# Kernel optimization log

Measured on AMD Instinct MI355X. Metric: run time of the kernel, lower is better.

Reference implementation:

```python
import jax, jax.numpy as jnp
import numpy as np
from jax import lax

CONF_THRESH = 0.01
IOU_THRESH = 0.45
TOP_K = 200
NMS_MAX = 400        # nms_max_output_size
NMS_CAND = 512       # candidates kept per class before greedy NMS (fixed-shape cap)
IMG_H = 512.0
IMG_W = 512.0
BATCH, N_BOXES, N_CLASSES = 32, 8732, 81  # last dim = N_CLASSES + 12


def setup_inputs() -> dict:
    key = jax.random.key(0)
    y_pred = jax.random.uniform(key, (BATCH, N_BOXES, N_CLASSES + 12), dtype=jnp.float32)
    return {"y_pred": y_pred}


def _decode_boxes(y):
    # centroids decode: offsets * variances * anchors + anchor centers
    anchor_w = y[..., -6]
    anchor_h = y[..., -5]
    cx = y[..., -12] * y[..., -4] * anchor_w + y[..., -8]
    cy = y[..., -11] * y[..., -3] * anchor_h + y[..., -7]
    w = jnp.exp(y[..., -10] * y[..., -2]) * anchor_w
    h = jnp.exp(y[..., -9] * y[..., -1]) * anchor_h
    xmin = (cx - 0.5 * w) * IMG_W  # normalize_coords=True -> scale to absolute
    ymin = (cy - 0.5 * h) * IMG_H
    xmax = (cx + 0.5 * w) * IMG_W
    ymax = (cy + 0.5 * h) * IMG_H
    return jnp.stack([xmin, ymin, xmax, ymax], axis=-1)  # (B,N,4)


def _iou(box, boxes):
    # box: (...,1,4) vs boxes: (...,K,4), coords [xmin,ymin,xmax,ymax]
    ix1 = jnp.maximum(box[..., 0], boxes[..., 0])
    iy1 = jnp.maximum(box[..., 1], boxes[..., 1])
    ix2 = jnp.minimum(box[..., 2], boxes[..., 2])
    iy2 = jnp.minimum(box[..., 3], boxes[..., 3])
    inter = jnp.maximum(ix2 - ix1, 0.0) * jnp.maximum(iy2 - iy1, 0.0)
    area_a = (box[..., 2] - box[..., 0]) * (box[..., 3] - box[..., 1])
    area_b = (boxes[..., 2] - boxes[..., 0]) * (boxes[..., 3] - boxes[..., 1])
    union = area_a + area_b - inter
    return jnp.where(union > 0, inter / union, 0.0)


def _forward(y_pred):
    B, N, D = y_pred.shape
    C = D - 12 - 1  # foreground classes (class 0 = background is skipped)
    K = NMS_CAND
    boxes = _decode_boxes(y_pred)                        # (B,N,4)
    scores = jnp.swapaxes(y_pred[..., 1:D - 12], 1, 2)   # (B,C,N)
    valid = scores > CONF_THRESH

    # sort candidates per (batch, class) by score desc; invalid go last
    order = jnp.argsort(jnp.where(valid, -scores, jnp.inf), axis=-1)[..., :K]
    s_s = jnp.take_along_axis(scores, order, axis=-1)            # (B,C,K)
    v_s = jnp.take_along_axis(valid, order, axis=-1)             # (B,C,K)
    boxes_bc = jnp.broadcast_to(boxes[:, None], (B, C, N, 4))
    b_s = jnp.take_along_axis(boxes_bc, order[..., None], axis=2)  # (B,C,K,4)

    # greedy NMS over sorted candidates, batched over (B,C)
    def step(carry, x):
        suppressed, count = carry  # (B,C,K) bool, (B,C) int32
        v_i, box_i, i = x
        sup_i = lax.dynamic_index_in_dim(suppressed, i, axis=2, keepdims=False)
        keep = v_i & ~sup_i & (count < NMS_MAX)
        iou = _iou(box_i[:, :, None, :], b_s)            # (B,C,K)
        later = jnp.arange(K) > i
        suppressed = suppressed | (keep[..., None] & (iou > IOU_THRESH) & later)
        return (suppressed, count + keep.astype(jnp.int32)), keep

    init = (jnp.zeros((B, C, K), bool), jnp.zeros((B, C), jnp.int32))
    xs = (jnp.moveaxis(v_s, 2, 0), jnp.moveaxis(b_s, 2, 0), jnp.arange(K))
    _, keeps = lax.scan(step, init, xs)
    keep = jnp.moveaxis(keeps, 0, 2)  # (B,C,K)

    # rows: [class_id, confidence, xmin, ymin, xmax, ymax]
    cls_ids = jnp.broadcast_to((jnp.arange(C, dtype=jnp.float32) + 1.0)[None, :, None], (B, C, K))
    entries = jnp.concatenate([cls_ids[..., None], s_s[..., None], b_s], axis=-1)  # (B,C,K,6)

    # compact kept rows to the front of each class block, zero-pad to NMS_MAX
    pos = jnp.where(keep, jnp.cumsum(keep, axis=-1) - 1, NMS_MAX)  # OOB -> dropped
    bb = jnp.arange(B)[:, None, None]
    cc = jnp.arange(C)[None, :, None]
    padded = jnp.zeros((B, C, NMS_MAX, 6), jnp.float32).at[bb, cc, pos].set(entries, mode='drop')

    flat = padded.reshape(B, C * NMS_MAX, 6)
    _, idx = lax.top_k(flat[:, :, 1], TOP_K)
    return jnp.take_along_axis(flat, idx[:, :, None], axis=1)  # (B, TOP_K, 6)


def reference(y_pred):
    return _forward(y_pred)
```

## Files before the change

kernel.cpp:

```cpp
#include <hip/hip_runtime.h>
#include <stdint.h>


#define BATCH   32
#define NBOX    8732
#define NCH     93
#define NCLS    80
#define KSEL    512
#define NMSMAX  400
#define RPC     200
#define TOPK    200
#define CONF    0.01f
#define IOU_T   0.45f
#define NPT     35

#define M_IOU   0.45000000298023223876953125

typedef unsigned long long u64;
typedef unsigned int       u32;

__device__ __forceinline__ u32 forder(float f) {
  u32 u = __float_as_uint(f);
  return u ^ ((u >> 31) ? 0xFFFFFFFFu : 0x80000000u);
}

template<int NN, int T>
__device__ void bsort(u64* s, int tid, bool asc) {
  for (int k = 2; k <= NN; k <<= 1) {
    for (int j = k >> 1; j > 0; j >>= 1) {
      __syncthreads();
      for (int i = tid; i < NN; i += T) {
        int p = i ^ j;
        if (p > i) {
          u64 a = s[i], b = s[p];
          bool up = (((i & k) == 0) == asc);
          if (up ? (a > b) : (a < b)) { s[i] = b; s[p] = a; }
        }
      }
    }
  }
  __syncthreads();
}

template<int NN, int T>
__device__ void bmerge_asc(u64* s, int tid) {
  for (int j = NN >> 1; j > 0; j >>= 1) {
    __syncthreads();
    for (int i = tid; i < NN; i += T) {
      int p = i ^ j;
      if (p > i) {
        u64 a = s[i], b = s[p];
        if (a > b) { s[i] = b; s[p] = a; }
      }
    }
  }
  __syncthreads();
}

__global__ __launch_bounds__(256) void decode_transpose(
    const float* __restrict__ y, float4* __restrict__ boxes, float* __restrict__ scoresT) {
  __shared__ float tile[64 * NCH];
  int b  = blockIdx.x;
  int t0 = blockIdx.y * 64;
  int nn = NBOX - t0; if (nn > 64) nn = 64;
  const float* src = y + ((size_t)b * NBOX + t0) * NCH;
  int tid = threadIdx.x;
  for (int i = tid; i < nn * NCH; i += 256) tile[i] = src[i];
  __syncthreads();
  if (tid < nn) {
    const float* yy = &tile[tid * NCH];
    float aw = yy[87], ah = yy[88];
    float cx = __fadd_rn(__fmul_rn(__fmul_rn(yy[81], yy[89]), aw), yy[85]);
    float cy = __fadd_rn(__fmul_rn(__fmul_rn(yy[82], yy[90]), ah), yy[86]);
    float w  = __fmul_rn(expf(__fmul_rn(yy[83], yy[91])), aw);
    float h  = __fmul_rn(expf(__fmul_rn(yy[84], yy[92])), ah);
    float4 bx;
    bx.x = __fmul_rn(__fsub_rn(cx, __fmul_rn(0.5f, w)), 512.0f);
    bx.y = __fmul_rn(__fsub_rn(cy, __fmul_rn(0.5f, h)), 512.0f);
    bx.z = __fmul_rn(__fadd_rn(cx, __fmul_rn(0.5f, w)), 512.0f);
    bx.w = __fmul_rn(__fadd_rn(cy, __fmul_rn(0.5f, h)), 512.0f);
    boxes[(size_t)b * NBOX + t0 + tid] = bx;
  }
  for (int e = tid; e < NCLS * 64; e += 256) {
    int c = e >> 6, ln = e & 63;
    if (ln < nn)
      scoresT[((size_t)b * NCLS + c) * NBOX + t0 + ln] = tile[ln * NCH + 1 + c];
  }
}

__global__ __launch_bounds__(256) void select_top512(
    const float* __restrict__ scoresT, u64* __restrict__ selkeys) {
  __shared__ u32 hist[256];
  __shared__ u64 cand[1024];
  __shared__ u32 bcast[4];
  int bc  = blockIdx.x;
  int t   = threadIdx.x;
  const float* sc = scoresT + (size_t)bc * NBOX;
  int base = t * NPT;
  int cnt  = NBOX - base; cnt = cnt < 0 ? 0 : (cnt > NPT ? NPT : cnt);

  u32 khi[NPT];
  #pragma unroll
  for (int k = 0; k < NPT; ++k) {
    float s = (k < cnt) ? sc[base + k] : 0.0f;
    u32 f = forder(s);
    khi[k] = ((k < cnt) && (s > CONF)) ? ~f : 0xFFFFFFFFu;
  }

  u32 prefix = 0, cntLess = 0, cntTie = 0;
  int shift = 24, p;
  for (p = 0; p < 4; ++p) {
    shift = 24 - 8 * p;
    __syncthreads();
    hist[t] = 0;
    __syncthreads();
    #pragma unroll
    for (int k = 0; k < NPT; ++k) {
      u32 x = khi[k];
      bool match = (p == 0) || ((x >> (shift + 8)) == prefix);
      if (match) atomicAdd(&hist[(x >> shift) & 0xFFu], 1u);
    }
    __syncthreads();
    if (t < 64) {
      u32 h0 = hist[4*t], h1 = hist[4*t+1], h2 = hist[4*t+2], h3 = hist[4*t+3];
      u32 lsum = h0 + h1 + h2 + h3;
      u32 scn = lsum;
      #pragma unroll
      for (int d = 1; d < 64; d <<= 1) {
        u32 v = __shfl_up(scn, d, 64);
        if (t >= d) scn += v;
      }
      u32 before = scn - lsum;
      u32 need = 512u - cntLess;
      u32 c0 = before + h0, c1 = c0 + h1, c2 = c1 + h2, c3 = c2 + h3;
      int bin = -1; u32 cb = 0;
      if (before < need) {
        if      (c0 >= need) { bin = 4*t;     cb = before; }
        else if (c1 >= need) { bin = 4*t + 1; cb = c0; }
        else if (c2 >= need) { bin = 4*t + 2; cb = c1; }
        else if (c3 >= need) { bin = 4*t + 3; cb = c2; }
      }
      if (bin >= 0) { bcast[0] = (u32)bin; bcast[1] = cb; }
    }
    __syncthreads();
    u32 bin = bcast[0];
    prefix  = (prefix << 8) | bin;
    cntLess += bcast[1];
    cntTie  = hist[bin];
    if (cntLess + cntTie <= 1024u) break;
  }

  if (p < 4) {
    __syncthreads();
    if (t == 0) bcast[2] = 0;
    __syncthreads();
    #pragma unroll
    for (int k = 0; k < NPT; ++k) {
      u32 x = khi[k];
      if ((x >> shift) <= prefix) {
        u32 pos = atomicAdd(&bcast[2], 1u);
        cand[pos] = ((u64)x << 32) | (u32)(base + k);
      }
    }
    __syncthreads();
    u32 m = bcast[2];
    for (int i = t; i < 1024; i += 256) if (i >= (int)m) cand[i] = ~0ULL;
    bsort<1024, 256>(cand, t, true);
    for (int i = t; i < KSEL; i += 256) selkeys[(size_t)bc * KSEL + i] = cand[i];
  } else {
    u32 V = prefix;
    __syncthreads();
    if (t == 0) bcast[2] = 0;
    __syncthreads();
    #pragma unroll
    for (int k = 0; k < NPT; ++k) {
      u32 x = khi[k];
      if (x < V) {
        u32 pos = atomicAdd(&bcast[2], 1u);
        cand[pos] = ((u64)x << 32) | (u32)(base + k);
      }
    }
    __syncthreads();
    u32 m = bcast[2];
    for (int i = t; i < 512; i += 256) if (i >= (int)m) cand[i] = ~0ULL;
    bsort<512, 256>(cand, t, true);
    for (int i = t; i < (int)m; i += 256) selkeys[(size_t)bc * KSEL + i] = cand[i];
    u32 myeq = 0;
    #pragma unroll
    for (int k = 0; k < NPT; ++k) if (khi[k] == V) myeq++;
    __syncthreads();
    hist[t] = myeq;
    __syncthreads();
    for (int d = 1; d < 256; d <<= 1) {
      u32 v = hist[t];
      u32 w = (t >= d) ? hist[t - d] : 0u;
      __syncthreads();
      hist[t] = v + w;
      __syncthreads();
    }
    u32 r = hist[t] - myeq;
    u32 needEq = 512u - m;
    #pragma unroll
    for (int k = 0; k < NPT; ++k) {
      if (khi[k] == V) {
        if (r < needEq)
          selkeys[(size_t)bc * KSEL + m + r] = ((u64)V << 32) | (u32)(base + k);
        r++;
      }
    }
  }
}

__global__ __launch_bounds__(256) void nms(
    const u64* __restrict__ selkeys, const float4* __restrict__ boxes,
    float* __restrict__ rows, u64* __restrict__ keys) {
  __shared__ float4 sbox[KSEL];
  __shared__ float  sarea[KSEL];
  __shared__ float  sscore[KSEL];
  __shared__ unsigned char svalid[KSEL];
  __shared__ u64   cmat[64][8];
  __shared__ short skidx[RPC];
  __shared__ int   s_gcount;
  int bc = blockIdx.x;
  int b = bc / NCLS, c = bc % NCLS;
  int tid = threadIdx.x;

  for (int i = tid; i < KSEL; i += 256) {
    u64 k  = selkeys[(size_t)bc * KSEL + i];
    u32 khi = (u32)(k >> 32);
    u32 idx = (u32)k;
    bool val = (khi != 0xFFFFFFFFu);
    u32 x = ~khi;
    u32 bits = (x & 0x80000000u) ? (x ^ 0x80000000u) : ~x;
    sscore[i] = __uint_as_float(bits);
    svalid[i] = val ? 1 : 0;
    float4 bx = make_float4(0.f, 0.f, 0.f, 0.f);
    if (val && idx < NBOX) bx = boxes[(size_t)b * NBOX + idx];
    sbox[i] = bx;
    sarea[i] = __fmul_rn(__fsub_rn(bx.z, bx.x), __fsub_rn(bx.w, bx.y));
  }
  if (tid == 0) s_gcount = 0;
  __syncthreads();

  u64 keptm[8] = {0,0,0,0,0,0,0,0};

  #pragma unroll
  for (int T = 0; T < 8; ++T) {
    bool active = (s_gcount < RPC);
    if (active) {
      for (int task = tid; task < 64 * (T + 1); task += 256) {
        int jl = task & 63, wi = task >> 6;
        int j = T * 64 + jl;
        float4 bj = sbox[j];
        float ab = sarea[j];
        u64 m = 0;
        for (int ii = 0; ii < 64; ++ii) {
          int i = wi * 64 + ii;
          float4 bi = sbox[i];
          float aa = sarea[i];
          float ix1 = fmaxf(bi.x, bj.x);
          float iy1 = fmaxf(bi.y, bj.y);
          float ix2 = fminf(bi.z, bj.z);
          float iy2 = fminf(bi.w, bj.w);
          float iw = fmaxf(__fsub_rn(ix2, ix1), 0.f);
          float ih = fmaxf(__fsub_rn(iy2, iy1), 0.f);
          float inter = __fmul_rn(iw, ih);
          float un = __fsub_rn(__fadd_rn(aa, ab), inter);
          bool s = (un > 0.f) && ((double)inter > M_IOU * (double)un);
          m |= ((u64)(s ? 1u : 0u)) << ii;
        }
        cmat[jl][wi] = m;
      }
    }
    __syncthreads();
    if (active && tid < 64) {
      int lane = tid;
      u64 cm[8];
      #pragma unroll
      for (int w = 0; w < 8; ++w) cm[w] = (w <= T) ? cmat[lane][w] : 0ull;
      int count = s_gcount;
      u64 hit = 0;
      #pragma unroll
      for (int w = 0; w < 8; ++w) hit |= cm[w] & keptm[w];
      bool valb = (svalid[T * 64 + lane] != 0);
      u64 alive = __ballot(valb && (hit == 0ull));
      while (alive != 0ull && count < RPC) {
        int i = __ffsll(alive) - 1;
        if (lane == i) skidx[count] = (short)(T * 64 + i);
        keptm[T] |= (1ull << i);
        alive &= ~(1ull << i);
        count++;
        if (count >= RPC) break;
        bool ks = ((cm[T] >> i) & 1ull) != 0ull;
        alive &= ~__ballot(ks);
      }
      if (lane == 0) s_gcount = count;
    }
    __syncthreads();
  }

  int count = s_gcount;
  for (int r = tid; r < RPC; r += 256) {
    float* row = rows + ((size_t)bc * RPC + r) * 6;
    u64 k;
    if (r < count) {
      int i = skidx[r];
      float s = sscore[i];
      float4 bx = sbox[i];
      row[0] = (float)(c + 1); row[1] = s;
      row[2] = bx.x; row[3] = bx.y; row[4] = bx.z; row[5] = bx.w;
      k = ((u64)(~forder(s)) << 32) | (u32)(c * NMSMAX + r);
    } else {
      row[0] = 0.f; row[1] = 0.f; row[2] = 0.f; row[3] = 0.f; row[4] = 0.f; row[5] = 0.f;
      k = ((u64)0x7FFFFFFFu << 32) | (u32)(c * NMSMAX + r);
    }
    keys[(size_t)bc * RPC + r] = k;
  }
}

__global__ __launch_bounds__(256) void topk_l1(
    const u64* __restrict__ keys, u64* __restrict__ out1) {
  __shared__ u64 buf[256], chk[256];
  int b = blockIdx.x, g = blockIdx.y;
  const u64* kb = keys + (size_t)b * (NCLS * RPC) + (size_t)g * (8 * RPC);
  int tid = threadIdx.x;
  buf[tid] = kb[tid];
  bsort<256, 256>(buf, tid, true);
  for (int c0 = 256; c0 < 1792; c0 += 256) {
    int n = c0 + tid;
    chk[tid] = (n < 8 * RPC) ? kb[n] : ~0ULL;
    bsort<256, 256>(chk, tid, false);
    u64 a = buf[tid], bb = chk[tid];
    buf[tid] = (a < bb) ? a : bb;
    bmerge_asc<256, 256>(buf, tid);
  }
  out1[((size_t)b * 10 + g) * 256 + tid] = buf[tid];
}

__global__ __launch_bounds__(256) void topk_l2(
    const u64* __restrict__ out1, const float* __restrict__ rows, float* __restrict__ out) {
  __shared__ u64 buf[256], chk[256];
  int b = blockIdx.x;
  const u64* kb = out1 + (size_t)b * 2560;
  int tid = threadIdx.x;
  buf[tid] = kb[tid];
  bsort<256, 256>(buf, tid, true);
  for (int c0 = 256; c0 < 2560; c0 += 256) {
    chk[tid] = kb[c0 + tid];
    bsort<256, 256>(chk, tid, false);
    u64 a = buf[tid], bb = chk[tid];
    buf[tid] = (a < bb) ? a : bb;
    bmerge_asc<256, 256>(buf, tid);
  }
  if (tid < TOPK) {
    u64 k = buf[tid];
    u32 f = (u32)k;
    float* o = out + ((size_t)b * TOPK + tid) * 6;
    if (f == 0xFFFFFFFFu) {
      o[0]=0.f; o[1]=0.f; o[2]=0.f; o[3]=0.f; o[4]=0.f; o[5]=0.f;
    } else {
      u32 c = f / NMSMAX;
      u32 r = f % NMSMAX;
      const float* row = rows + (((size_t)b * NCLS + c) * RPC + r) * 6;
      o[0]=row[0]; o[1]=row[1]; o[2]=row[2]; o[3]=row[3]; o[4]=row[4]; o[5]=row[5];
    }
  }
}

extern "C" void kernel_launch(void* const* d_in, const int* in_sizes, int n_in,
                              void* d_out, int out_size, void* d_ws, size_t ws_size,
                              hipStream_t stream) {
  (void)in_sizes; (void)n_in; (void)out_size; (void)ws_size;
  const float* y = (const float*)d_in[0];
  float* out = (float*)d_out;
  char* ws = (char*)d_ws;

  constexpr size_t OFF_BOXES   = 0;
  constexpr size_t SZ_BOXES    = (size_t)BATCH * NBOX * 4 * 4;
  constexpr size_t OFF_SCORES  = OFF_BOXES + SZ_BOXES;
  constexpr size_t SZ_SCORES   = (size_t)BATCH * NCLS * NBOX * 4;
  constexpr size_t OFF_SELKEYS = OFF_SCORES + SZ_SCORES;
  constexpr size_t SZ_SELKEYS  = (size_t)BATCH * NCLS * KSEL * 8;
  constexpr size_t OFF_ROWS    = OFF_SELKEYS + SZ_SELKEYS;
  constexpr size_t SZ_ROWS     = (size_t)BATCH * NCLS * RPC * 6 * 4;
  constexpr size_t OFF_KEYS    = OFF_ROWS + SZ_ROWS;
  constexpr size_t SZ_KEYS     = (size_t)BATCH * NCLS * RPC * 8;
  constexpr size_t OFF_OUT1    = OFF_KEYS + SZ_KEYS;

  float4* boxes  = (float4*)(ws + OFF_BOXES);
  float* scoresT = (float*)(ws + OFF_SCORES);
  u64* selkeys   = (u64*)(ws + OFF_SELKEYS);
  float* rows    = (float*)(ws + OFF_ROWS);
  u64* keys      = (u64*)(ws + OFF_KEYS);
  u64* out1      = (u64*)(ws + OFF_OUT1);

  dim3 gA(BATCH, (NBOX + 63) / 64);
  decode_transpose<<<gA, 256, 0, stream>>>(y, boxes, scoresT);
  select_top512<<<BATCH * NCLS, 256, 0, stream>>>(scoresT, selkeys);
  nms<<<BATCH * NCLS, 256, 0, stream>>>(selkeys, boxes, rows, keys);
  dim3 gD1(BATCH, 10);
  topk_l1<<<gD1, 256, 0, stream>>>(keys, out1);
  topk_l2<<<BATCH, 256, 0, stream>>>(out1, rows, out);
}
```

Measured before the change: 691.9 us.

## Check NMS candidates only against kept boxes instead of full IoU matrix

Reworks the per-class NMS block. Each 64-candidate tile is now tested only against the already-kept boxes, split across four waves and combined by ballot, plus a 64x64 intra-tile IoU mask built in 16-bit chunks. Previously each tile computed IoU against every earlier candidate. Box data moves from float4 to structure-of-arrays in shared memory, and the loop exits early once 200 boxes are kept. This cuts IoU work from quadratic in candidates to roughly candidates times kept boxes, but the loop over kept boxes is serial and uneven across waves.

```diff
diff --git a/kernel.cpp b/kernel.cpp
--- a/kernel.cpp
+++ b/kernel.cpp
@@ -22,6 +22,20 @@
 __device__ __forceinline__ u32 forder(float f) {
   u32 u = __float_as_uint(f);
   return u ^ ((u >> 31) ? 0xFFFFFFFFu : 0x80000000u);
+}
+
+__device__ __forceinline__ bool iou_gt(
+    float kx, float ky, float kz, float kw, float aa,
+    float bx, float by, float bz, float bw, float ab) {
+  float ix1 = fmaxf(kx, bx);
+  float iy1 = fmaxf(ky, by);
+  float ix2 = fminf(kz, bz);
+  float iy2 = fminf(kw, bw);
+  float iw = fmaxf(__fsub_rn(ix2, ix1), 0.f);
+  float ih = fmaxf(__fsub_rn(iy2, iy1), 0.f);
+  float inter = __fmul_rn(iw, ih);
+  float un = __fsub_rn(__fadd_rn(aa, ab), inter);
+  return (un > 0.f) && ((double)inter > M_IOU * (double)un);
 }
 
 template<int NN, int T>
@@ -214,13 +228,12 @@
 __global__ __launch_bounds__(256) void nms(
     const u64* __restrict__ selkeys, const float4* __restrict__ boxes,
     float* __restrict__ rows, u64* __restrict__ keys) {
-  __shared__ float4 sbox[KSEL];
-  __shared__ float  sarea[KSEL];
-  __shared__ float  sscore[KSEL];
+  __shared__ float sx[KSEL], sy[KSEL], sz[KSEL], sw_[KSEL], sa[KSEL], ss[KSEL];
   __shared__ unsigned char svalid[KSEL];
-  __shared__ u64   cmat[64][8];
   __shared__ short skidx[RPC];
   __shared__ int   s_gcount;
+  __shared__ u64   ssup[4];
+  __shared__ u32   scmat[64][5];
   int bc = blockIdx.x;
   int b = bc / NCLS, c = bc % NCLS;
   int tid = threadIdx.x;
@@ -232,69 +245,60 @@
     bool val = (khi != 0xFFFFFFFFu);
     u32 x = ~khi;
     u32 bits = (x & 0x80000000u) ? (x ^ 0x80000000u) : ~x;
-    sscore[i] = __uint_as_float(bits);
+    ss[i] = __uint_as_float(bits);
     svalid[i] = val ? 1 : 0;
     float4 bx = make_float4(0.f, 0.f, 0.f, 0.f);
     if (val && idx < NBOX) bx = boxes[(size_t)b * NBOX + idx];
-    sbox[i] = bx;
-    sarea[i] = __fmul_rn(__fsub_rn(bx.z, bx.x), __fsub_rn(bx.w, bx.y));
+    sx[i] = bx.x; sy[i] = bx.y; sz[i] = bx.z; sw_[i] = bx.w;
+    sa[i] = __fmul_rn(__fsub_rn(bx.z, bx.x), __fsub_rn(bx.w, bx.y));
   }
   if (tid == 0) s_gcount = 0;
   __syncthreads();
 
-  u64 keptm[8] = {0,0,0,0,0,0,0,0};
-
-  #pragma unroll
+  int jl = tid & 63, wv = tid >> 6;
   for (int T = 0; T < 8; ++T) {
-    bool active = (s_gcount < RPC);
-    if (active) {
-      for (int task = tid; task < 64 * (T + 1); task += 256) {
-        int jl = task & 63, wi = task >> 6;
-        int j = T * 64 + jl;
-        float4 bj = sbox[j];
-        float ab = sarea[j];
-        u64 m = 0;
-        for (int ii = 0; ii < 64; ++ii) {
-          int i = wi * 64 + ii;
-          float4 bi = sbox[i];
-          float aa = sarea[i];
-          float ix1 = fmaxf(bi.x, bj.x);
-          float iy1 = fmaxf(bi.y, bj.y);
-          float ix2 = fminf(bi.z, bj.z);
-          float iy2 = fminf(bi.w, bj.w);
-          float iw = fmaxf(__fsub_rn(ix2, ix1), 0.f);
-          float ih = fmaxf(__fsub_rn(iy2, iy1), 0.f);
-          float inter = __fmul_rn(iw, ih);
-          float un = __fsub_rn(__fadd_rn(aa, ab), inter);
-          bool s = (un > 0.f) && ((double)inter > M_IOU * (double)un);
-          m |= ((u64)(s ? 1u : 0u)) << ii;
-        }
-        cmat[jl][wi] = m;
-      }
-    }
-    __syncthreads();
-    if (active && tid < 64) {
+    int count = s_gcount;
+    if (count >= RPC) break;
+    int j = T * 64 + jl;
+    float bjx = sx[j], bjy = sy[j], bjz = sz[j], bjw = sw_[j], ab = sa[j];
+
+    bool supA = false;
+    for (int r = wv; r < count; r += 4) {
+      int ki = skidx[r];
+      if (iou_gt(sx[ki], sy[ki], sz[ki], sw_[ki], sa[ki], bjx, bjy, bjz, bjw, ab))
+        supA = true;
+    }
+    u64 bwm = __ballot(supA);
+    if (jl == 0) ssup[wv] = bwm;
+
+    u32 mchunk = 0;
+    #pragma unroll
+    for (int k = 0; k < 16; ++k) {
+      int i = T * 64 + wv * 16 + k;
+      bool s = iou_gt(sx[i], sy[i], sz[i], sw_[i], sa[i], bjx, bjy, bjz, bjw, ab);
+      mchunk |= (s ? 1u : 0u) << k;
+    }
+    scmat[jl][wv] = mchunk;
+    __syncthreads();
+
+    if (tid < 64) {
       int lane = tid;
-      u64 cm[8];
-      #pragma unroll
-      for (int w = 0; w < 8; ++w) cm[w] = (w <= T) ? cmat[lane][w] : 0ull;
-      int count = s_gcount;
-      u64 hit = 0;
-      #pragma unroll
-      for (int w = 0; w < 8; ++w) hit |= cm[w] & keptm[w];
+      u64 cm = (u64)scmat[lane][0] | ((u64)scmat[lane][1] << 16)
+             | ((u64)scmat[lane][2] << 32) | ((u64)scmat[lane][3] << 48);
+      u64 supm = ssup[0] | ssup[1] | ssup[2] | ssup[3];
       bool valb = (svalid[T * 64 + lane] != 0);
-      u64 alive = __ballot(valb && (hit == 0ull));
-      while (alive != 0ull && count < RPC) {
+      u64 alive = __ballot(valb && !((supm >> lane) & 1ull));
+      int cnt = count;
+      while (alive != 0ull && cnt < RPC) {
         int i = __ffsll(alive) - 1;
-        if (lane == i) skidx[count] = (short)(T * 64 + i);
-        keptm[T] |= (1ull << i);
+        if (lane == 0) skidx[cnt] = (short)(T * 64 + i);
         alive &= ~(1ull << i);
-        count++;
-        if (count >= RPC) break;
-        bool ks = ((cm[T] >> i) & 1ull) != 0ull;
+        cnt++;
+        if (cnt >= RPC) break;
+        bool ks = ((cm >> i) & 1ull) != 0ull;
         alive &= ~__ballot(ks);
       }
-      if (lane == 0) s_gcount = count;
+      if (lane == 0) s_gcount = cnt;
     }
     __syncthreads();
   }
@@ -305,10 +309,9 @@
     u64 k;
     if (r < count) {
       int i = skidx[r];
-      float s = sscore[i];
-      float4 bx = sbox[i];
+      float s = ss[i];
       row[0] = (float)(c + 1); row[1] = s;
-      row[2] = bx.x; row[3] = bx.y; row[4] = bx.z; row[5] = bx.w;
+      row[2] = sx[i]; row[3] = sy[i]; row[4] = sz[i]; row[5] = sw_[i];
       k = ((u64)(~forder(s)) << 32) | (u32)(c * NMSMAX + r);
     } else {
       row[0] = 0.f; row[1] = 0.f; row[2] = 0.f; row[3] = 0.f; row[4] = 0.f; row[5] = 0.f;
```

Measured after the change: 613.5 us. 1.13x faster.
